# Kernel tuning notes

Hardware: AMD Instinct MI355X
Metric: run time of the kernel (lower is better)

## Reference

```python
import jax, jax.numpy as jnp
import numpy as np

BS, C_IN, CTX, TGT = 2, 8, 1024, 96
D_MODEL, N_HEADS, D_FF, N_LAYERS = 256, 16, 1024, 4
PF, SF, PC, SC = 8, 4, 32, 16
NF = (CTX + SF - PF) // SF + 1   # 256 fine patches (incl. end-pad)
NC = (CTX + SC - PC) // SC + 1   # 64 coarse patches
TOTAL = NF + NC                  # 320
EPS = 1e-5
DK = D_MODEL // N_HEADS
SCALE = DK ** -0.5


def _patchify(z, plen, stride):
    # ReplicationPad1d((0, stride)) then unfold -> (bs, c, n_patches, plen)
    pad = jnp.broadcast_to(z[..., -1:], z.shape[:-1] + (stride,))
    zp = jnp.concatenate([z, pad], axis=-1)
    n = (zp.shape[-1] - plen) // stride + 1
    idx = np.arange(n)[:, None] * stride + np.arange(plen)[None, :]
    return zp[..., idx]


def _layernorm(x, s, b):
    m = x.mean(-1, keepdims=True)
    v = jnp.var(x, axis=-1, keepdims=True)
    return (x - m) * jax.lax.rsqrt(v + EPS) * s + b


def setup_inputs() -> dict:
    key = jax.random.key(0)
    ks = jax.random.split(key, 16)
    g = lambda k, shape: jax.random.normal(k, shape, jnp.float32) * 0.02
    return {
        "z": jax.random.normal(ks[0], (BS, C_IN, CTX), jnp.float32),
        "revin_w": jnp.ones((C_IN,), jnp.float32),
        "revin_b": jnp.zeros((C_IN,), jnp.float32),
        "Wf": g(ks[1], (PF, D_MODEL)), "bf": jnp.zeros((D_MODEL,), jnp.float32),
        "Wc": g(ks[2], (PC, D_MODEL)), "bc": jnp.zeros((D_MODEL,), jnp.float32),
        "W_pos": jax.random.uniform(ks[3], (TOTAL, D_MODEL), jnp.float32, -0.02, 0.02),
        "WQ": g(ks[4], (N_LAYERS, D_MODEL, D_MODEL)), "bQ": jnp.zeros((N_LAYERS, D_MODEL), jnp.float32),
        "WK": g(ks[5], (N_LAYERS, D_MODEL, D_MODEL)), "bK": jnp.zeros((N_LAYERS, D_MODEL), jnp.float32),
        "WV": g(ks[6], (N_LAYERS, D_MODEL, D_MODEL)), "bV": jnp.zeros((N_LAYERS, D_MODEL), jnp.float32),
        "WO": g(ks[7], (N_LAYERS, D_MODEL, D_MODEL)), "bO": jnp.zeros((N_LAYERS, D_MODEL), jnp.float32),
        "ln1_s": jnp.ones((N_LAYERS, D_MODEL), jnp.float32), "ln1_b": jnp.zeros((N_LAYERS, D_MODEL), jnp.float32),
        "ln2_s": jnp.ones((N_LAYERS, D_MODEL), jnp.float32), "ln2_b": jnp.zeros((N_LAYERS, D_MODEL), jnp.float32),
        "F1": g(ks[8], (N_LAYERS, D_MODEL, D_FF)), "c1": jnp.zeros((N_LAYERS, D_FF), jnp.float32),
        "F2": g(ks[9], (N_LAYERS, D_FF, D_MODEL)), "c2": jnp.zeros((N_LAYERS, D_MODEL), jnp.float32),
        "Wh": g(ks[10], (D_MODEL * TOTAL, TGT)), "bh": jnp.zeros((TGT,), jnp.float32),
    }


def reference(z, revin_w, revin_b, Wf, bf, Wc, bc, W_pos, WQ, bQ, WK, bK, WV, bV,
              WO, bO, ln1_s, ln1_b, ln2_s, ln2_b, F1, c1, F2, c2, Wh, bh):
    # RevIN norm over the time axis (last axis of (bs, c, T))
    mean = z.mean(-1, keepdims=True)
    std = jnp.sqrt(jnp.var(z, axis=-1, keepdims=True) + EPS)
    zn = (z - mean) / std * revin_w[None, :, None] + revin_b[None, :, None]

    # dual-scale patch embedding
    x_fine = _patchify(zn, PF, SF) @ Wf + bf      # (bs, c, NF, d)
    x_coarse = _patchify(zn, PC, SC) @ Wc + bc    # (bs, c, NC, d)
    x = jnp.concatenate([x_fine, x_coarse], axis=2)  # (bs, c, TOTAL, d)

    u = x.reshape(BS * C_IN, TOTAL, D_MODEL) + W_pos  # (B, S, d), B=bs*c

    # residual-score transformer encoder (post-norm)
    prev = None
    for l in range(N_LAYERS):
        q = (u @ WQ[l] + bQ[l]).reshape(-1, TOTAL, N_HEADS, DK).transpose(0, 2, 1, 3)
        k = (u @ WK[l] + bK[l]).reshape(-1, TOTAL, N_HEADS, DK).transpose(0, 2, 1, 3)
        v = (u @ WV[l] + bV[l]).reshape(-1, TOTAL, N_HEADS, DK).transpose(0, 2, 1, 3)
        s = jnp.einsum('bhqd,bhkd->bhqk', q, k) * SCALE
        if prev is not None:
            s = s + prev
        w = jax.nn.softmax(s, axis=-1)
        o = jnp.einsum('bhqk,bhkd->bhqd', w, v).transpose(0, 2, 1, 3).reshape(-1, TOTAL, D_MODEL)
        o = o @ WO[l] + bO[l]
        u = _layernorm(u + o, ln1_s[l], ln1_b[l])
        h = jax.nn.gelu(u @ F1[l] + c1[l], approximate=False) @ F2[l] + c2[l]
        u = _layernorm(u + h, ln2_s[l], ln2_b[l])
        prev = s

    # head: (bs, c, TOTAL, d) -> permute -> flatten(d, TOTAL) -> linear
    zz = u.reshape(BS, C_IN, TOTAL, D_MODEL).transpose(0, 1, 3, 2).reshape(BS, C_IN, D_MODEL * TOTAL)
    out = zz @ Wh + bh  # (bs, c, TGT)

    # RevIN denorm
    out = (out - revin_b[None, :, None]) / (revin_w[None, :, None] + EPS * EPS) * std + mean
    return out
```

## Files before the change

### kernel.cpp

```cpp
#include <hip/hip_runtime.h>
#include <math.h>

typedef unsigned short ushort;
typedef unsigned int uint;
typedef __attribute__((ext_vector_type(8))) short short8;
typedef __attribute__((ext_vector_type(4))) float f32x4;
typedef __attribute__((ext_vector_type(4))) ushort us4;

constexpr int BS = 2, C_IN = 8, CTX = 1024, TGT = 96;
constexpr int DM = 256, NH = 16, DFF = 1024, NL = 4;
constexpr int NF = 256, TOTAL = 320;
constexpr int NB = 16;
constexpr int DK = 16;
constexpr float EPS = 1e-5f;
constexpr float SCALE = 0.25f;
constexpr int KHEAD = DM * TOTAL;
constexpr int M = NB * TOTAL;

__device__ __forceinline__ ushort f2b(float x) {
    uint u = __float_as_uint(x);
    u += 0x7fff + ((u >> 16) & 1);
    return (ushort)(u >> 16);
}
__device__ __forceinline__ float bu2f(ushort x) { return __uint_as_float(((uint)x) << 16); }
__device__ __forceinline__ uint pack2(float a, float b) { return (uint)f2b(a) | ((uint)f2b(b) << 16); }

typedef __attribute__((address_space(3))) uint lds_u32;
typedef const __attribute__((address_space(1))) uint glb_u32;
__device__ __forceinline__ void ldst16(const void* g, void* l) {
    __builtin_amdgcn_global_load_lds((glb_u32*)g, (lds_u32*)l, 16, 0, 0);
}

#define PIPE_BARRIER() asm volatile("s_waitcnt vmcnt(0)\n\ts_barrier" ::: "memory")

__global__ __launch_bounds__(256) void k_prep(
        const float* __restrict__ WQ, const float* __restrict__ WK,
        const float* __restrict__ WV, const float* __restrict__ WO,
        const float* __restrict__ F1, const float* __restrict__ F2,
        const float* __restrict__ Wh,
        ushort* __restrict__ Wtqkv, ushort* __restrict__ WtO,
        ushort* __restrict__ Ft1, ushort* __restrict__ Ft2,
        ushort* __restrict__ WhT2,
        const float* __restrict__ z, const float* __restrict__ rw,
        const float* __restrict__ rb,
        const float* __restrict__ Wf, const float* __restrict__ bfv,
        const float* __restrict__ Wc, const float* __restrict__ bcv,
        const float* __restrict__ Wpos, ushort* __restrict__ u,
        const float* __restrict__ bhv, float* __restrict__ outp,
        float* __restrict__ scalef) {
    __shared__ __align__(16) ushort tile[64 * 98];
    __shared__ float szn[CTX];
    __shared__ float red1[4], red2[4];
    int i = blockIdx.x, tid = threadIdx.x;

    if (i < 768) {
        const float* src; ushort* dst; int lsrc, ldst_, r0, c0;
        if (i < 256) {
            int mat = i >> 4, l = mat >> 2, w = mat & 3;
            src = (w == 0 ? WQ : (w == 1 ? WK : (w == 2 ? WV : WO))) + l * 65536;
            dst = (w < 3) ? (Wtqkv + (size_t)l * 768 * 256 + w * 65536)
                          : (WtO + (size_t)l * 65536);
            lsrc = 256; ldst_ = 256; r0 = ((i >> 2) & 3) * 64; c0 = (i & 3) * 64;
        } else if (i < 512) {
            int j = i - 256, l = j >> 6, t = j & 63;
            src = F1 + (size_t)l * 262144; dst = Ft1 + (size_t)l * 262144;
            lsrc = 1024; ldst_ = 256; r0 = (t >> 4) * 64; c0 = (t & 15) * 64;
        } else {
            int j = i - 512, l = j >> 6, t = j & 63;
            src = F2 + (size_t)l * 262144; dst = Ft2 + (size_t)l * 262144;
            lsrc = 256; ldst_ = 1024; r0 = (t >> 2) * 64; c0 = (t & 3) * 64;
        }
#pragma unroll
        for (int it = 0; it < 4; it++) {
            int fid = it * 256 + tid;
            int fr = fid >> 4, fc = fid & 15;
            f32x4 v = *(const f32x4*)&src[(size_t)(r0 + fr) * lsrc + c0 + fc * 4];
            ushort* tr = &tile[fr * 66];
            tr[fc * 4 + 0] = f2b(v[0]); tr[fc * 4 + 1] = f2b(v[1]);
            tr[fc * 4 + 2] = f2b(v[2]); tr[fc * 4 + 3] = f2b(v[3]);
        }
        __syncthreads();
#pragma unroll
        for (int it = 0; it < 4; it++) {
            int sid = it * 256 + tid;
            int cr = sid >> 4, cc = sid & 15;
            us4 v = (us4){ tile[(cc * 4 + 0) * 66 + cr], tile[(cc * 4 + 1) * 66 + cr],
                           tile[(cc * 4 + 2) * 66 + cr], tile[(cc * 4 + 3) * 66 + cr] };
            *(us4*)&dst[(size_t)(c0 + cr) * ldst_ + r0 + cc * 4] = v;
        }
    } else if (i < 2048) {
        int j = i - 768;
        int pp = j >> 2, d0 = (j & 3) * 64;
#pragma unroll
        for (int it = 0; it < 6; it++) {
            int fid = it * 256 + tid;
            int fr = fid / 24, fc = fid % 24;
            f32x4 v = *(const f32x4*)&Wh[((size_t)(d0 + fr) * 320 + pp) * 96 + fc * 4];
            ushort* tr = &tile[fr * 98];
            tr[fc * 4 + 0] = f2b(v[0]); tr[fc * 4 + 1] = f2b(v[1]);
            tr[fc * 4 + 2] = f2b(v[2]); tr[fc * 4 + 3] = f2b(v[3]);
        }
        __syncthreads();
#pragma unroll
        for (int it = 0; it < 6; it++) {
            int sid = it * 256 + tid;
            int tr = sid >> 4, dc = sid & 15;
            us4 v = (us4){ tile[(dc * 4 + 0) * 98 + tr], tile[(dc * 4 + 1) * 98 + tr],
                           tile[(dc * 4 + 2) * 98 + tr], tile[(dc * 4 + 3) * 98 + tr] };
            *(us4*)&WhT2[(size_t)tr * KHEAD + pp * 256 + d0 + dc * 4] = v;
        }
    } else {
        int j = i - 2048;
        int bc = j / 80, pb = j % 80;
        int wave = tid >> 6, lane = tid & 63;
        f32x4 zv = *(const f32x4*)&z[bc * CTX + tid * 4];
        float s1 = zv[0] + zv[1] + zv[2] + zv[3];
        float s2 = zv[0] * zv[0] + zv[1] * zv[1] + zv[2] * zv[2] + zv[3] * zv[3];
#pragma unroll
        for (int off = 1; off < 64; off <<= 1) {
            s1 += __shfl_xor(s1, off);
            s2 += __shfl_xor(s2, off);
        }
        if (lane == 0) { red1[wave] = s1; red2[wave] = s2; }
        __syncthreads();
        s1 = red1[0] + red1[1] + red1[2] + red1[3];
        s2 = red2[0] + red2[1] + red2[2] + red2[3];
        float m = s1 * (1.0f / CTX);
        float var = s2 * (1.0f / CTX) - m * m;
        float sd = sqrtf(var + EPS);
        int c = bc & 7;
        float w = rw[c], bb = rb[c];
        float inv_sd_w = w / sd;
#pragma unroll
        for (int k = 0; k < 4; k++) szn[tid * 4 + k] = (zv[k] - m) * inv_sd_w + bb;
        if (pb == 0) {
            if (tid < TGT) outp[bc * TGT + tid] = (bhv[tid] - bb) / (w + EPS * EPS) * sd + m;
            if (tid == 0) scalef[bc] = sd / (w + EPS * EPS);
        }
        __syncthreads();
#pragma unroll
        for (int pi = 0; pi < 4; pi++) {
            int p = pb * 4 + pi, d = tid;
            float acc;
            if (p < NF) {
                acc = bfv[d];
                int base = p * 4;
#pragma unroll
                for (int q = 0; q < 8; q++)
                    acc += szn[min(base + q, CTX - 1)] * Wf[q * DM + d];
            } else {
                acc = bcv[d];
                int base = (p - NF) * 16;
#pragma unroll
                for (int q = 0; q < 32; q++)
                    acc += szn[min(base + q, CTX - 1)] * Wc[q * DM + d];
            }
            acc += Wpos[p * DM + d];
            u[((size_t)bc * TOTAL + p) * DM + d] = f2b(acc);
        }
    }
}

template <int GELU, int QKV>
__global__ __launch_bounds__(256) void k_gemm_mfma(const ushort* __restrict__ A,
                                                   const ushort* __restrict__ Wt,
                                                   const float* __restrict__ b0,
                                                   const float* __restrict__ b1,
                                                   const float* __restrict__ b2,
                                                   ushort* __restrict__ C,
                                                   ushort* __restrict__ C2,
                                                   int Mm, int N, int K) {
    __shared__ ushort As[2][64][32];
    __shared__ ushort Bs[2][64][32];
    int tid = threadIdx.x;
    int wave = tid >> 6, lane = tid & 63;
    int quad = lane >> 4, l16 = lane & 15;
    int m0 = blockIdx.y * 64, n0 = blockIdx.x * 64;

    f32x4 acc[4];
#pragma unroll
    for (int nt = 0; nt < 4; nt++) acc[nt] = (f32x4){0.f, 0.f, 0.f, 0.f};

    int srow = wave * 16 + (lane >> 2);
    int sc = (lane & 3) ^ ((srow >> 1) & 3);
    const ushort* Ag = &A[(size_t)(m0 + srow) * K + sc * 8];
    const ushort* Bg = &Wt[(size_t)(n0 + srow) * K + sc * 8];
    int rchunk = (quad ^ ((l16 >> 1) & 3)) * 8;

    ldst16(Ag, &As[0][wave * 16][0]);
    ldst16(Bg, &Bs[0][wave * 16][0]);
    PIPE_BARRIER();

    int nstep = K >> 5;
    int cur = 0;
    for (int t = 0; t < nstep; t++) {
        if (t + 1 < nstep) {
            ldst16(Ag + (t + 1) * 32, &As[cur ^ 1][wave * 16][0]);
            ldst16(Bg + (t + 1) * 32, &Bs[cur ^ 1][wave * 16][0]);
        }
        short8 af = *(const short8*)&As[cur][wave * 16 + l16][rchunk];
#pragma unroll
        for (int nt = 0; nt < 4; nt++) {
            short8 bf = *(const short8*)&Bs[cur][nt * 16 + l16][rchunk];
            acc[nt] = __builtin_amdgcn_mfma_f32_16x16x32_bf16(af, bf, acc[nt], 0, 0, 0);
        }
        PIPE_BARRIER();
        cur ^= 1;
    }
#pragma unroll
    for (int nt = 0; nt < 4; nt++) {
        int col = n0 + nt * 16 + l16;
        float bi;
        if (QKV) {
            int bs = (n0 + nt * 16) >> 8;
            const float* bp = bs == 0 ? b0 : (bs == 1 ? b1 : b2);
            bi = bp[col & 255];
        } else {
            bi = b0[col];
        }
#pragma unroll
        for (int r = 0; r < 4; r++) {
            int rowm = m0 + wave * 16 + quad * 4 + r;
            float vv = acc[nt][r] + bi;
            if (GELU) vv = vv * 0.5f * (1.0f + erff(vv * 0.70710678118f));
            if (QKV) {
                int bs = col >> 8;
                int c = col & 255, hh = c >> 4, d = c & 15;
                ushort* dst = (bs == 2) ? C2 : (C + (size_t)bs * (M * DM));
                dst[(size_t)hh * (M * DK) + (size_t)rowm * DK + d] = f2b(vv);
            } else {
                C[(size_t)rowm * N + col] = f2b(vv);
            }
        }
    }
}

__global__ __launch_bounds__(256) void k_gemm_ln16(const ushort* __restrict__ A,
                                                   const ushort* __restrict__ Wt,
                                                   const float* __restrict__ bias,
                                                   const float* __restrict__ ls,
                                                   const float* __restrict__ lb,
                                                   ushort* __restrict__ u, int K) {
    __shared__ ushort As[2][16][32];
    __shared__ ushort Bs[2][256][32];
    __shared__ float ps1[16][4], ps2[16][4];
    int tid = threadIdx.x;
    int wave = tid >> 6, lane = tid & 63;
    int quad = lane >> 4, l16 = lane & 15;
    int m0 = blockIdx.x * 16;

    f32x4 acc[4];
#pragma unroll
    for (int nt = 0; nt < 4; nt++) acc[nt] = (f32x4){0.f, 0.f, 0.f, 0.f};

    int brow = wave * 16 + (lane >> 2);
    int bc_swz = (lane & 3) ^ ((brow >> 1) & 3);
    const ushort* Bg0 = &Wt[(size_t)brow * K + bc_swz * 8];
    int ar = lane >> 2;
    int ac = (lane & 3) ^ ((ar >> 1) & 3);
    const ushort* Ag = &A[(size_t)(m0 + ar) * K + ac * 8];
    int rchunk = (quad ^ ((l16 >> 1) & 3)) * 8;

    if (tid < 64) ldst16(Ag, &As[0][0][0]);
#pragma unroll
    for (int i = 0; i < 4; i++)
        ldst16(Bg0 + (size_t)i * 64 * K, &Bs[0][i * 64 + wave * 16][0]);
    PIPE_BARRIER();

    int nstep = K >> 5;
    int cur = 0;
    for (int t = 0; t < nstep; t++) {
        if (t + 1 < nstep) {
            if (tid < 64) ldst16(Ag + (t + 1) * 32, &As[cur ^ 1][0][0]);
#pragma unroll
            for (int i = 0; i < 4; i++)
                ldst16(Bg0 + (size_t)i * 64 * K + (t + 1) * 32, &Bs[cur ^ 1][i * 64 + wave * 16][0]);
        }
        short8 af = *(const short8*)&As[cur][l16][rchunk];
#pragma unroll
        for (int nt = 0; nt < 4; nt++) {
            short8 bf = *(const short8*)&Bs[cur][wave * 64 + nt * 16 + l16][rchunk];
            acc[nt] = __builtin_amdgcn_mfma_f32_16x16x32_bf16(af, bf, acc[nt], 0, 0, 0);
        }
        PIPE_BARRIER();
        cur ^= 1;
    }
    float xv[4][4];
#pragma unroll
    for (int r = 0; r < 4; r++) {
        int rowg = m0 + quad * 4 + r;
        float s1 = 0.f, s2 = 0.f;
#pragma unroll
        for (int nt = 0; nt < 4; nt++) {
            int col = wave * 64 + nt * 16 + l16;
            float x = acc[nt][r] + bias[col] + bu2f(u[(size_t)rowg * DM + col]);
            xv[r][nt] = x; s1 += x; s2 += x * x;
        }
        s1 += __shfl_xor(s1, 1); s2 += __shfl_xor(s2, 1);
        s1 += __shfl_xor(s1, 2); s2 += __shfl_xor(s2, 2);
        s1 += __shfl_xor(s1, 4); s2 += __shfl_xor(s2, 4);
        s1 += __shfl_xor(s1, 8); s2 += __shfl_xor(s2, 8);
        if (l16 == 0) { ps1[quad * 4 + r][wave] = s1; ps2[quad * 4 + r][wave] = s2; }
    }
    __syncthreads();
#pragma unroll
    for (int r = 0; r < 4; r++) {
        int rowl = quad * 4 + r, rowg = m0 + rowl;
        float s1 = ps1[rowl][0] + ps1[rowl][1] + ps1[rowl][2] + ps1[rowl][3];
        float s2 = ps2[rowl][0] + ps2[rowl][1] + ps2[rowl][2] + ps2[rowl][3];
        float m = s1 * (1.0f / DM);
        float var = s2 * (1.0f / DM) - m * m;
        float rs = rsqrtf(var + EPS);
#pragma unroll
        for (int nt = 0; nt < 4; nt++) {
            int col = wave * 64 + nt * 16 + l16;
            u[(size_t)rowg * DM + col] = f2b((xv[r][nt] - m) * rs * ls[col] + lb[col]);
        }
    }
}

__global__ __launch_bounds__(256, 4) void k_attn(const ushort* __restrict__ qk, const ushort* __restrict__ vm,
                                                 ushort* __restrict__ ao, int nj) {
    __shared__ ushort sh[15360];
    uint* sh32 = (uint*)sh;
    int bh = blockIdx.x, b = bh >> 4, h = bh & 15;
    int i0 = blockIdx.y * 64;
    int t = threadIdx.x, wave = t >> 6, lane = t & 63, quad = lane >> 4, l16 = lane & 15;
    const short8 zero8 = (short8){0, 0, 0, 0, 0, 0, 0, 0};
    size_t hplane = (size_t)h * (M * DK) + (size_t)b * TOTAL * DK;

    f32x4 acc[20];
#pragma unroll
    for (int nt = 0; nt < 20; nt++) acc[nt] = (f32x4){0.f, 0.f, 0.f, 0.f};

    for (int idx = t; idx < 320; idx += 256) {
        int jp = idx >> 1, dh = idx & 1;
        int j = jp * 2;
        uint4 a = *(const uint4*)&vm[hplane + (size_t)j * DK + dh * 8];
        uint4 bb = *(const uint4*)&vm[hplane + (size_t)(j + 1) * DK + dh * 8];
        const ushort* ap = (const ushort*)&a;
        const ushort* bp = (const ushort*)&bb;
        int jr = j & 31;
        int q = (jr & 15) >> 2, jj = ((jr >> 4) << 2) + (jr & 3);
        int base = 10240 + ((j >> 5) * 4 + q) * 128 + jj;
#pragma unroll
        for (int dd = 0; dd < 8; dd++) {
            int d = dh * 8 + dd;
            uint val = (uint)ap[dd] | ((uint)bp[dd] << 16);
            sh32[(base + d * 8) >> 1] = val;
        }
    }

    for (int jl = 0; jl < nj; jl++) {
        const ushort* qm = qk + (size_t)(2 * jl) * M * DM;
        const ushort* km = qm + (size_t)M * DM;
        int kb = (jl & 1) * 5120;
        for (int idx = t; idx < 640; idx += 256) {
            int j = idx >> 1, half = idx & 1;
            short8 kv = *(const short8*)&km[hplane + (size_t)idx * 8];
            int jt = j >> 4, jln = j & 15;
            *(short8*)&sh[kb + ((jt * 2 + half) * 16 + jln) * 8] = kv;
        }
        short8 qf = zero8;
        if (quad < 2) qf = *(const short8*)&qm[hplane + (size_t)(i0 + wave * 16 + l16) * DK + quad * 8];
        __syncthreads();
#pragma unroll
        for (int nt = 0; nt < 20; nt++) {
            short8 kf = *(const short8*)&sh[kb + ((nt * 2 + (quad & 1)) * 16 + l16) * 8];
            acc[nt] = __builtin_amdgcn_mfma_f32_16x16x32_bf16(kf, qf, acc[nt], 0, 0, 0);
        }
    }

    float mx = -1e30f;
#pragma unroll
    for (int nt = 0; nt < 20; nt++)
#pragma unroll
        for (int r = 0; r < 4; r++) { acc[nt][r] *= SCALE; mx = fmaxf(mx, acc[nt][r]); }
    mx = fmaxf(mx, __shfl_xor(mx, 16));
    mx = fmaxf(mx, __shfl_xor(mx, 32));
    float sum = 0.f;
#pragma unroll
    for (int nt = 0; nt < 20; nt++)
#pragma unroll
        for (int r = 0; r < 4; r++) { acc[nt][r] = __expf(acc[nt][r] - mx); sum += acc[nt][r]; }
    sum += __shfl_xor(sum, 16);
    sum += __shfl_xor(sum, 32);
    float inv = 1.f / sum;
#pragma unroll
    for (int nt = 0; nt < 20; nt++)
#pragma unroll
        for (int r = 0; r < 4; r++) acc[nt][r] *= inv;

    f32x4 oacc = (f32x4){0.f, 0.f, 0.f, 0.f};
#pragma unroll
    for (int jt2 = 0; jt2 < 10; jt2++) {
        short8 vt = *(const short8*)&sh[10240 + ((jt2 * 4 + quad) * 16 + l16) * 8];
        union { short8 v; uint u[4]; } pf;
        pf.u[0] = pack2(acc[2 * jt2][0], acc[2 * jt2][1]);
        pf.u[1] = pack2(acc[2 * jt2][2], acc[2 * jt2][3]);
        pf.u[2] = pack2(acc[2 * jt2 + 1][0], acc[2 * jt2 + 1][1]);
        pf.u[3] = pack2(acc[2 * jt2 + 1][2], acc[2 * jt2 + 1][3]);
        oacc = __builtin_amdgcn_mfma_f32_16x16x32_bf16(vt, pf.v, oacc, 0, 0, 0);
    }
    us4 ov4 = (us4){f2b(oacc[0]), f2b(oacc[1]), f2b(oacc[2]), f2b(oacc[3])};
    *(us4*)&ao[((size_t)b * TOTAL + i0 + wave * 16 + l16) * DM + h * DK + quad * 4] = ov4;
}

__global__ __launch_bounds__(256) void k_head(const ushort* __restrict__ u, const ushort* __restrict__ WhT2,
                                              const float* __restrict__ scalef, float* __restrict__ out) {
    int t0 = blockIdx.x * 16;
    int wave = threadIdx.x >> 6, lane = threadIdx.x & 63;
    int quad = lane >> 4, l16 = lane & 15;
    int chunk = blockIdx.y * 4 + wave;
    int kbeg = chunk * 1024;
    f32x4 acc = (f32x4){0.f, 0.f, 0.f, 0.f};
    const ushort* za = &u[(size_t)l16 * KHEAD + quad * 8];
    const ushort* wb = &WhT2[(size_t)(t0 + l16) * KHEAD + quad * 8];
#pragma unroll 4
    for (int k = kbeg; k < kbeg + 1024; k += 32) {
        short8 af = *(const short8*)&za[k];
        short8 bf = *(const short8*)&wb[k];
        acc = __builtin_amdgcn_mfma_f32_16x16x32_bf16(af, bf, acc, 0, 0, 0);
    }
#pragma unroll
    for (int r = 0; r < 4; r++) {
        int bcr = quad * 4 + r;
        atomicAdd(&out[bcr * TGT + t0 + l16], acc[r] * scalef[bcr]);
    }
}

extern "C" void kernel_launch(void* const* d_in, const int* in_sizes, int n_in,
                              void* d_out, int out_size, void* d_ws, size_t ws_size,
                              hipStream_t stream) {
    const float* z       = (const float*)d_in[0];
    const float* revin_w = (const float*)d_in[1];
    const float* revin_b = (const float*)d_in[2];
    const float* Wf      = (const float*)d_in[3];
    const float* bfv     = (const float*)d_in[4];
    const float* Wc      = (const float*)d_in[5];
    const float* bcv     = (const float*)d_in[6];
    const float* Wpos    = (const float*)d_in[7];
    const float* WQ      = (const float*)d_in[8];
    const float* bQ      = (const float*)d_in[9];
    const float* WK      = (const float*)d_in[10];
    const float* bK      = (const float*)d_in[11];
    const float* WV      = (const float*)d_in[12];
    const float* bV      = (const float*)d_in[13];
    const float* WO      = (const float*)d_in[14];
    const float* bO      = (const float*)d_in[15];
    const float* ln1s    = (const float*)d_in[16];
    const float* ln1b    = (const float*)d_in[17];
    const float* ln2s    = (const float*)d_in[18];
    const float* ln2b    = (const float*)d_in[19];
    const float* F1      = (const float*)d_in[20];
    const float* c1      = (const float*)d_in[21];
    const float* F2      = (const float*)d_in[22];
    const float* c2      = (const float*)d_in[23];
    const float* Wh      = (const float*)d_in[24];
    const float* bh      = (const float*)d_in[25];
    float* out = (float*)d_out;

    char* p = (char*)d_ws;
    float* scalef = (float*)p;   p += 16 * 4;
    p = (char*)(((size_t)p + 255) & ~255ull);
    ushort* u     = (ushort*)p;  p += (size_t)M * DM * 2;
    ushort* qkbuf = (ushort*)p;  p += (size_t)NL * 2 * M * DM * 2;
    ushort* vbuf  = (ushort*)p;  p += (size_t)M * DM * 2;
    ushort* ax    = (ushort*)p;  p += (size_t)M * DM * 2;
    ushort* hbuf  = (ushort*)p;  p += (size_t)M * DFF * 2;
    ushort* Wtqkv = (ushort*)p;  p += (size_t)NL * 768 * 256 * 2;
    ushort* WtO   = (ushort*)p;  p += (size_t)NL * 256 * 256 * 2;
    ushort* Ft1   = (ushort*)p;  p += (size_t)NL * 1024 * 256 * 2;
    ushort* Ft2   = (ushort*)p;  p += (size_t)NL * 256 * 1024 * 2;
    ushort* WhT2  = (ushort*)p;  p += (size_t)TGT * KHEAD * 2;

    k_prep<<<3328, 256, 0, stream>>>(WQ, WK, WV, WO, F1, F2, Wh,
                                     Wtqkv, WtO, Ft1, Ft2, WhT2,
                                     z, revin_w, revin_b,
                                     Wf, bfv, Wc, bcv, Wpos, u,
                                     bh, out, scalef);

    for (int l = 0; l < NL; l++) {
        k_gemm_mfma<0, 1><<<dim3(12, 80), 256, 0, stream>>>(
            u, Wtqkv + (size_t)l * 768 * 256, bQ + l * DM, bK + l * DM, bV + l * DM,
            qkbuf + (size_t)l * 2 * M * DM, vbuf, M, 768, 256);
        k_attn<<<dim3(NB * NH, 5), 256, 0, stream>>>(qkbuf, vbuf, ax, l + 1);
        k_gemm_ln16<<<M / 16, 256, 0, stream>>>(
            ax, WtO + (size_t)l * 65536, bO + l * DM, ln1s + l * DM, ln1b + l * DM, u, 256);
        k_gemm_mfma<1, 0><<<dim3(16, 80), 256, 0, stream>>>(
            u, Ft1 + (size_t)l * 262144, c1 + l * DFF, c1, c1, hbuf, hbuf, M, 1024, 256);
        k_gemm_ln16<<<M / 16, 256, 0, stream>>>(
            hbuf, Ft2 + (size_t)l * 262144, c2 + l * DM, ln2s + l * DM, ln2b + l * DM, u, 1024);
    }

    k_head<<<dim3(TGT / 16, 20), 256, 0, stream>>>(u, WhT2, scalef, out);
}
```

Measured before the change: 427.7 us.

## Pre-swizzle K/V in QKV epilogue and bulk-load all attention tiles upfront

The QKV GEMM epilogue now writes K and V directly in the MFMA-friendly swizzled layouts the attention kernel expects, so the attention kernel can copy them into LDS with contiguous 16-byte loads (ldst16) instead of per-element transposing stores. All K tiles for every accumulated layer plus V are loaded once, with a single barrier, instead of one barrier per layer. Q fragments are prefetched into registers, and setprio is raised around the MFMA loops. LDS use grows from about 30KB to 50KB and occupancy drops from 4 to 3 blocks per CU; the epilogue's scattered writes get a bit more index arithmetic.

```diff
diff --git a/kernel.cpp b/kernel.cpp
--- a/kernel.cpp
+++ b/kernel.cpp
@@ -226,8 +226,18 @@
             if (QKV) {
                 int bs = col >> 8;
                 int c = col & 255, hh = c >> 4, d = c & 15;
-                ushort* dst = (bs == 2) ? C2 : (C + (size_t)bs * (M * DM));
-                dst[(size_t)hh * (M * DK) + (size_t)rowm * DK + d] = f2b(vv);
+                int bb = rowm / 320, j = rowm - bb * 320;
+                size_t plane = (size_t)hh * (M * DK) + (size_t)bb * (TOTAL * DK);
+                if (bs == 0) {
+                    C[plane + (size_t)j * DK + d] = f2b(vv);
+                } else if (bs == 1) {
+                    int off = (((j >> 4) * 2 + (d >> 3)) * 16 + (j & 15)) * 8 + (d & 7);
+                    C[(size_t)M * DM + plane + off] = f2b(vv);
+                } else {
+                    int off = ((j >> 5) * 4 + ((j & 15) >> 2)) * 128 +
+                              (((j >> 4) & 1) << 2) + (j & 3) + d * 8;
+                    C2[plane + off] = f2b(vv);
+                }
             } else {
                 C[(size_t)rowm * N + col] = f2b(vv);
             }
@@ -319,57 +329,50 @@
     }
 }
 
-__global__ __launch_bounds__(256, 4) void k_attn(const ushort* __restrict__ qk, const ushort* __restrict__ vm,
+__global__ __launch_bounds__(256, 3) void k_attn(const ushort* __restrict__ qk, const ushort* __restrict__ vm,
                                                  ushort* __restrict__ ao, int nj) {
-    __shared__ ushort sh[15360];
-    uint* sh32 = (uint*)sh;
+    __shared__ __align__(16) ushort sh[25600];
     int bh = blockIdx.x, b = bh >> 4, h = bh & 15;
     int i0 = blockIdx.y * 64;
     int t = threadIdx.x, wave = t >> 6, lane = t & 63, quad = lane >> 4, l16 = lane & 15;
     const short8 zero8 = (short8){0, 0, 0, 0, 0, 0, 0, 0};
-    size_t hplane = (size_t)h * (M * DK) + (size_t)b * TOTAL * DK;
+    size_t hplane = (size_t)h * (M * DK) + (size_t)b * (TOTAL * DK);
+
+    int nchunks = (nj + 1) * 10;
+    for (int c = wave; c < nchunks; c += 4) {
+        int s = c / 10, cc = c - s * 10;
+        const ushort* src = (s < nj)
+            ? qk + (size_t)(2 * s + 1) * (M * DM) + hplane + cc * 512
+            : vm + hplane + cc * 512;
+        int dstbase = (s < nj ? s * 5120 : 20480) + cc * 512;
+        ldst16(src + lane * 8, &sh[dstbase]);
+    }
+    short8 qfr[4] = { zero8, zero8, zero8, zero8 };
+    int qrow = i0 + wave * 16 + l16;
+#pragma unroll
+    for (int jl = 0; jl < 4; jl++)
+        if (jl < nj && quad < 2)
+            qfr[jl] = *(const short8*)&qk[(size_t)(2 * jl) * (M * DM) + hplane +
+                                          (size_t)qrow * DK + quad * 8];
+    PIPE_BARRIER();
 
     f32x4 acc[20];
 #pragma unroll
     for (int nt = 0; nt < 20; nt++) acc[nt] = (f32x4){0.f, 0.f, 0.f, 0.f};
 
-    for (int idx = t; idx < 320; idx += 256) {
-        int jp = idx >> 1, dh = idx & 1;
-        int j = jp * 2;
-        uint4 a = *(const uint4*)&vm[hplane + (size_t)j * DK + dh * 8];
-        uint4 bb = *(const uint4*)&vm[hplane + (size_t)(j + 1) * DK + dh * 8];
-        const ushort* ap = (const ushort*)&a;
-        const ushort* bp = (const ushort*)&bb;
-        int jr = j & 31;
-        int q = (jr & 15) >> 2, jj = ((jr >> 4) << 2) + (jr & 3);
-        int base = 10240 + ((j >> 5) * 4 + q) * 128 + jj;
-#pragma unroll
-        for (int dd = 0; dd < 8; dd++) {
-            int d = dh * 8 + dd;
-            uint val = (uint)ap[dd] | ((uint)bp[dd] << 16);
-            sh32[(base + d * 8) >> 1] = val;
-        }
-    }
-
-    for (int jl = 0; jl < nj; jl++) {
-        const ushort* qm = qk + (size_t)(2 * jl) * M * DM;
-        const ushort* km = qm + (size_t)M * DM;
-        int kb = (jl & 1) * 5120;
-        for (int idx = t; idx < 640; idx += 256) {
-            int j = idx >> 1, half = idx & 1;
-            short8 kv = *(const short8*)&km[hplane + (size_t)idx * 8];
-            int jt = j >> 4, jln = j & 15;
-            *(short8*)&sh[kb + ((jt * 2 + half) * 16 + jln) * 8] = kv;
-        }
-        short8 qf = zero8;
-        if (quad < 2) qf = *(const short8*)&qm[hplane + (size_t)(i0 + wave * 16 + l16) * DK + quad * 8];
-        __syncthreads();
-#pragma unroll
-        for (int nt = 0; nt < 20; nt++) {
-            short8 kf = *(const short8*)&sh[kb + ((nt * 2 + (quad & 1)) * 16 + l16) * 8];
-            acc[nt] = __builtin_amdgcn_mfma_f32_16x16x32_bf16(kf, qf, acc[nt], 0, 0, 0);
-        }
-    }
+    __builtin_amdgcn_s_setprio(1);
+#pragma unroll
+    for (int jl = 0; jl < 4; jl++) {
+        if (jl < nj) {
+            int kb = jl * 5120;
+#pragma unroll
+            for (int nt = 0; nt < 20; nt++) {
+                short8 kf = *(const short8*)&sh[kb + ((nt * 2 + (quad & 1)) * 16 + l16) * 8];
+                acc[nt] = __builtin_amdgcn_mfma_f32_16x16x32_bf16(kf, qfr[jl], acc[nt], 0, 0, 0);
+            }
+        }
+    }
+    __builtin_amdgcn_s_setprio(0);
 
     float mx = -1e30f;
 #pragma unroll
@@ -392,9 +395,10 @@
         for (int r = 0; r < 4; r++) acc[nt][r] *= inv;
 
     f32x4 oacc = (f32x4){0.f, 0.f, 0.f, 0.f};
+    __builtin_amdgcn_s_setprio(1);
 #pragma unroll
     for (int jt2 = 0; jt2 < 10; jt2++) {
-        short8 vt = *(const short8*)&sh[10240 + ((jt2 * 4 + quad) * 16 + l16) * 8];
+        short8 vt = *(const short8*)&sh[20480 + ((jt2 * 4 + quad) * 16 + l16) * 8];
         union { short8 v; uint u[4]; } pf;
         pf.u[0] = pack2(acc[2 * jt2][0], acc[2 * jt2][1]);
         pf.u[1] = pack2(acc[2 * jt2][2], acc[2 * jt2][3]);
@@ -402,6 +406,7 @@
         pf.u[3] = pack2(acc[2 * jt2 + 1][2], acc[2 * jt2 + 1][3]);
         oacc = __builtin_amdgcn_mfma_f32_16x16x32_bf16(vt, pf.v, oacc, 0, 0, 0);
     }
+    __builtin_amdgcn_s_setprio(0);
     us4 ov4 = (us4){f2b(oacc[0]), f2b(oacc[1]), f2b(oacc[2]), f2b(oacc[3])};
     *(us4*)&ao[((size_t)b * TOTAL + i0 + wave * 16 + l16) * DM + h * DK + quad * 4] = ov4;
 }
```

Measured after the change: 426.1 us. About the same (-0.4%).
